# Optimization experiments

Measured on AMD Instinct MI355X. Metric: run time of the kernel, lower is better.

## Reference

```python
import jax, jax.numpy as jnp
import numpy as np

D_MODEL = 1024
NUM_HEADS = 16
D_HEAD = D_MODEL // NUM_HEADS


def setup_inputs() -> dict:
    key = jax.random.key(0)
    ks = jax.random.split(key, 9)
    s = 1.0 / np.sqrt(D_MODEL)
    return {
        "x": jax.random.normal(ks[0], (2, 2048, D_MODEL), dtype=jnp.float32),
        "Wq": jax.random.normal(ks[1], (D_MODEL, D_MODEL), dtype=jnp.float32) * s,
        "bq": jnp.zeros((D_MODEL,), dtype=jnp.float32),
        "Wk": jax.random.normal(ks[2], (D_MODEL, D_MODEL), dtype=jnp.float32) * s,
        "bk": jnp.zeros((D_MODEL,), dtype=jnp.float32),
        "Wv": jax.random.normal(ks[3], (D_MODEL, D_MODEL), dtype=jnp.float32) * s,
        "bv": jnp.zeros((D_MODEL,), dtype=jnp.float32),
        "Wo": jax.random.normal(ks[4], (D_MODEL, D_MODEL), dtype=jnp.float32) * s,
        "bo": jnp.zeros((D_MODEL,), dtype=jnp.float32),
    }


def reference(x, Wq, bq, Wk, bk, Wv, bv, Wo, bo):
    B, S, D = x.shape
    H, Dh = NUM_HEADS, D_HEAD

    def split_heads(t):  # [B,S,D] -> [B,H,S,Dh]
        return t.reshape(B, S, H, Dh).transpose(0, 2, 1, 3)

    # Linear layers: y = x @ W^T + b (torch nn.Linear convention)
    Q = split_heads(x @ Wq.T + bq)
    K = split_heads(x @ Wk.T + bk)
    V = split_heads(x @ Wv.T + bv)

    scale = 1.0 / jnp.sqrt(jnp.asarray(Dh, dtype=x.dtype))
    scores = jnp.einsum("bhqd,bhkd->bhqk", Q, K) * scale  # [B,H,S,S]
    attn = jax.nn.softmax(scores, axis=-1)
    context = jnp.einsum("bhqk,bhkd->bhqd", attn, V)  # [B,H,S,Dh]
    context = context.transpose(0, 2, 1, 3).reshape(B, S, D)
    return context @ Wo.T + bo
```

## Files before the change

kernel.cpp:

```cpp
#include <hip/hip_runtime.h>


#define T_TOK 4096
#define DM    1024
#define SQ    2048
#define NH    16
#define DH    64

typedef unsigned short u16;
typedef unsigned int   u32;
typedef __bf16 bf16x8 __attribute__((ext_vector_type(8)));
typedef float  f32x4  __attribute__((ext_vector_type(4)));
typedef float  f32x16 __attribute__((ext_vector_type(16)));
typedef u32    u32x4  __attribute__((ext_vector_type(4)));

__device__ __forceinline__ u16 f2bf(float f) {
  u32 u = __builtin_bit_cast(u32, f);
  u32 r = (u + 0x7FFFu + ((u >> 16) & 1u)) >> 16;
  return (u16)r;
}

#if __has_builtin(__builtin_amdgcn_cvt_pk_bf16_f32)
typedef __bf16 bf16x2 __attribute__((ext_vector_type(2)));
__device__ __forceinline__ u32 pk2bf(float a, float b) {
  bf16x2 h = __builtin_amdgcn_cvt_pk_bf16_f32(a, b);
  return __builtin_bit_cast(u32, h);
}
#else
__device__ __forceinline__ u32 pk2bf(float a, float b) {
  u32 r;
  asm("v_cvt_pk_bf16_f32 %0, %1, %2" : "=v"(r) : "v"(a), "v"(b));
  return r;
}
#endif

__device__ __forceinline__ void gld16(const void* g, void* l) {
  __builtin_amdgcn_global_load_lds(
      (const __attribute__((address_space(1))) u32*)g,
      (__attribute__((address_space(3))) u32*)l, 16, 0, 0);
}

__global__ void cast_bf16_kernel(const float* __restrict__ x,
    const float* __restrict__ w0, const float* __restrict__ w1,
    const float* __restrict__ w2, const float* __restrict__ w3,
    u16* __restrict__ xb, u16* __restrict__ o0, u16* __restrict__ o1,
    u16* __restrict__ o2, u16* __restrict__ o3)
{
  const float* src; u16* dst; int n;
  switch (blockIdx.y) {
    case 0:  src = x;  dst = xb; n = T_TOK * DM; break;
    case 1:  src = w0; dst = o0; n = DM * DM; break;
    case 2:  src = w1; dst = o1; n = DM * DM; break;
    case 3:  src = w2; dst = o2; n = DM * DM; break;
    default: src = w3; dst = o3; n = DM * DM; break;
  }
  const int stride = gridDim.x * blockDim.x;
  for (int i = blockIdx.x * blockDim.x + threadIdx.x; i * 4 < n; i += stride) {
    float4 v = ((const float4*)src)[i];
    ushort4 o;
    o.x = f2bf(v.x); o.y = f2bf(v.y); o.z = f2bf(v.z); o.w = f2bf(v.w);
    ((ushort4*)dst)[i] = o;
  }
}

__device__ __forceinline__ void gemm_core_128x128(
    u16* lds, const u16* __restrict__ Ab, const u16* __restrict__ Bb,
    f32x4 acc[4][4])
{
  u16* As = lds;
  u16* Bs = lds + 8192;
  const int tid = threadIdx.x, lane = tid & 63, w = tid >> 6;
  const int waveM = w >> 1, waveN = w & 1;
  const int col = lane & 15, quad = lane >> 4;
  const int srow = lane >> 3;
  const int sg0  = (lane & 7) ^ srow;

  for (int k0 = 0; k0 < DM; k0 += 64) {
    #pragma unroll
    for (int i = 0; i < 4; ++i) {
      const int rb = w * 32 + i * 8;
      const int sg = sg0 ^ ((rb >> 3) & 3);
      gld16(Ab + (size_t)(rb + srow) * DM + k0 + sg * 8, &As[rb * 64]);
      gld16(Bb + (size_t)(rb + srow) * DM + k0 + sg * 8, &Bs[rb * 64]);
    }
    __syncthreads();
    #pragma unroll
    for (int c = 0; c < 2; ++c) {
      bf16x8 af[4], bg[4];
      #pragma unroll
      for (int i = 0; i < 4; ++i) {
        const int row = waveM * 64 + i * 16 + col;
        const int gp = (c * 4 + quad) ^ (row & 7) ^ ((row >> 3) & 3);
        af[i] = *(const bf16x8*)&As[row * 64 + gp * 8];
      }
      #pragma unroll
      for (int j = 0; j < 4; ++j) {
        const int row = waveN * 64 + j * 16 + col;
        const int gp = (c * 4 + quad) ^ (row & 7) ^ ((row >> 3) & 3);
        bg[j] = *(const bf16x8*)&Bs[row * 64 + gp * 8];
      }
      #pragma unroll
      for (int i = 0; i < 4; ++i) {
        #pragma unroll
        for (int j = 0; j < 4; ++j)
          acc[i][j] = __builtin_amdgcn_mfma_f32_16x16x32_bf16(af[i], bg[j], acc[i][j], 0, 0, 0);
      }
    }
    __syncthreads();
  }
}

__device__ __forceinline__ void gemm_core_128x64(
    u16* lds, const u16* __restrict__ Ab, const u16* __restrict__ Bb,
    f32x4 acc[4][2])
{
  u16* As = lds;
  u16* Bs = lds + 8192;
  const int tid = threadIdx.x, lane = tid & 63, w = tid >> 6;
  const int waveM = w >> 1, waveN = w & 1;
  const int col = lane & 15, quad = lane >> 4;
  const int srow = lane >> 3;
  const int sg0  = (lane & 7) ^ srow;

  for (int k0 = 0; k0 < DM; k0 += 64) {
    #pragma unroll
    for (int i = 0; i < 4; ++i) {
      const int rb = w * 32 + i * 8;
      const int sg = sg0 ^ ((rb >> 3) & 3);
      gld16(Ab + (size_t)(rb + srow) * DM + k0 + sg * 8, &As[rb * 64]);
    }
    #pragma unroll
    for (int i = 0; i < 2; ++i) {
      const int rb = w * 16 + i * 8;
      const int sg = sg0 ^ ((rb >> 3) & 3);
      gld16(Bb + (size_t)(rb + srow) * DM + k0 + sg * 8, &Bs[rb * 64]);
    }
    __syncthreads();
    #pragma unroll
    for (int c = 0; c < 2; ++c) {
      bf16x8 af[4], bg[2];
      #pragma unroll
      for (int i = 0; i < 4; ++i) {
        const int row = waveM * 64 + i * 16 + col;
        const int gp = (c * 4 + quad) ^ (row & 7) ^ ((row >> 3) & 3);
        af[i] = *(const bf16x8*)&As[row * 64 + gp * 8];
      }
      #pragma unroll
      for (int j = 0; j < 2; ++j) {
        const int row = waveN * 32 + j * 16 + col;
        const int gp = (c * 4 + quad) ^ (row & 7) ^ ((row >> 3) & 3);
        bg[j] = *(const bf16x8*)&Bs[row * 64 + gp * 8];
      }
      #pragma unroll
      for (int i = 0; i < 4; ++i) {
        #pragma unroll
        for (int j = 0; j < 2; ++j)
          acc[i][j] = __builtin_amdgcn_mfma_f32_16x16x32_bf16(af[i], bg[j], acc[i][j], 0, 0, 0);
      }
    }
    __syncthreads();
  }
}

__global__ __launch_bounds__(256) void gemm_qkv_kernel(
    const u16* __restrict__ xb,
    const u16* __restrict__ Wqb, const u16* __restrict__ Wkb, const u16* __restrict__ Wvb,
    const float* __restrict__ bq, const float* __restrict__ bk, const float* __restrict__ bv,
    u16* __restrict__ Qs, u16* __restrict__ Kh, u16* __restrict__ Vt)
{
  __shared__ __align__(16) u16 smem[128 * 136];
  u16* tr = smem;
  const int z = blockIdx.z;
  const int tb = blockIdx.x;
  const int cb = blockIdx.y;
  const u16*   Wb   = (z == 0) ? Wqb : (z == 1) ? Wkb : Wvb;
  const float* bias = (z == 0) ? bq  : (z == 1) ? bk  : bv;
  const float scale = (z == 0) ? 0.18033688011112042f : 1.0f;

  const int tid = threadIdx.x;
  const int lane = tid & 63, w = tid >> 6;
  const int waveM = w >> 1, waveN = w & 1;
  const int col = lane & 15, quad = lane >> 4;
  const f32x4 zf = {0.f, 0.f, 0.f, 0.f};

  f32x4 acc[4][4];
  #pragma unroll
  for (int i = 0; i < 4; ++i) {
    #pragma unroll
    for (int j = 0; j < 4; ++j) acc[i][j] = zf;
  }

  if (z == 2) {
    gemm_core_128x128(smem, xb + (size_t)(tb * 128) * DM,
                      Wb + (size_t)(cb * 128) * DM, acc);
    #pragma unroll
    for (int j = 0; j < 4; ++j) {
      const int cl = waveN * 64 + j * 16 + col;
      const float bb = bias[cb * 128 + cl];
      #pragma unroll
      for (int i = 0; i < 4; ++i) {
        const int tl = waveM * 64 + i * 16 + quad * 4;
        ushort4 pk;
        pk.x = f2bf(acc[i][j][0] + bb); pk.y = f2bf(acc[i][j][1] + bb);
        pk.z = f2bf(acc[i][j][2] + bb); pk.w = f2bf(acc[i][j][3] + bb);
        *(ushort4*)&tr[cl * 136 + tl] = pk;
      }
    }
    __syncthreads();
    const int t0 = tb * 128;
    const int b = t0 >> 11, sBase = t0 & 2047;
    #pragma unroll
    for (int rep = 0; rep < 8; ++rep) {
      const int chunk = rep * 256 + tid;
      const int row = chunk >> 4, off = (chunk & 15) * 8;
      const int c = cb * 128 + row;
      const int h = c >> 6, d = c & 63;
      uint4 v = *(const uint4*)&tr[row * 136 + off];
      *(uint4*)&Vt[((size_t)(b * NH + h) * DH + d) * SQ + sBase + off] = v;
    }
  } else {
    gemm_core_128x128(smem, Wb + (size_t)(cb * 128) * DM,
                      xb + (size_t)(tb * 128) * DM, acc);
    u16* out = (z == 0) ? Qs : Kh;
    const int chBase  = cb * 128 + waveM * 64;
    const int tokBase = tb * 128 + waveN * 64;
    #pragma unroll
    for (int i = 0; i < 4; ++i) {
      const int c0 = chBase + i * 16 + quad * 4;
      const int hh = c0 >> 6, d0 = c0 & 63;
      const float4 bb = *(const float4*)&bias[c0];
      #pragma unroll
      for (int j = 0; j < 4; ++j) {
        const int t = tokBase + j * 16 + col;
        const int b = t >> 11, s = t & 2047;
        ushort4 pk;
        pk.x = f2bf((acc[i][j][0] + bb.x) * scale);
        pk.y = f2bf((acc[i][j][1] + bb.y) * scale);
        pk.z = f2bf((acc[i][j][2] + bb.z) * scale);
        pk.w = f2bf((acc[i][j][3] + bb.w) * scale);
        *(ushort4*)&out[((size_t)(b * NH + hh) * SQ + s) * DH + d0] = pk;
      }
    }
  }
}

__global__ __launch_bounds__(256, 4) void attn_kernel(
    const u16* __restrict__ Qs, const u16* __restrict__ Kh,
    const u16* __restrict__ Vt, u16* __restrict__ ctx)
{
  __shared__ __align__(16) char smem[33 * 1024];
  u16* KtB = (u16*)smem;
  u16* VlB = (u16*)(smem + 16384);
  f32x4* red  = (f32x4*)smem;
  float* lred = (float*)(smem + 32768);

  const int tid = threadIdx.x, lane = tid & 63, w = tid >> 6;
  const int l31 = lane & 31, h = lane >> 5;
  const int qt = w & 1, st = w >> 1;
  const int bh = blockIdx.x, q0 = blockIdx.y * 64;
  const u16* Qb = Qs + ((size_t)bh * SQ + q0) * DH;
  const u16* Kb = Kh + (size_t)bh * SQ * DH;
  const u16* Vb = Vt + (size_t)bh * DH * SQ;
  const int srow = lane >> 3;
  const int sgl  = (lane & 7) ^ srow;

  bf16x8 qreg[4];
  #pragma unroll
  for (int ks = 0; ks < 4; ++ks)
    qreg[ks] = *(const bf16x8*)(Qb + (size_t)(qt * 32 + l31) * DH + ks * 16 + h * 8);

  #pragma unroll
  for (int i = 0; i < 2; ++i) {
    const int rb = w * 16 + i * 8;
    const int sg = sgl ^ ((rb >> 3) & 3);
    gld16(Kb + (size_t)(rb + srow) * DH + sg * 8, &KtB[rb * 64]);
    gld16(Vb + (size_t)(rb + srow) * SQ + sg * 8, &VlB[rb * 64]);
  }

  f32x16 cacc[2];
  #pragma unroll
  for (int dt = 0; dt < 2; ++dt)
    #pragma unroll
    for (int e = 0; e < 16; ++e) cacc[dt][e] = 0.f;
  float l_s = 0.f;
  __syncthreads();

  for (int kt = 0; kt < SQ / 64; ++kt) {
    const int cur = kt & 1;
    u16* Kt = KtB + cur * 4096;
    u16* Vl = VlB + cur * 4096;
    if (kt + 1 < SQ / 64) {
      const int nxt = cur ^ 1, s1 = (kt + 1) * 64;
      u16* Ktn = KtB + nxt * 4096;
      u16* Vln = VlB + nxt * 4096;
      #pragma unroll
      for (int i = 0; i < 2; ++i) {
        const int rb = w * 16 + i * 8;
        const int sg = sgl ^ ((rb >> 3) & 3);
        gld16(Kb + (size_t)(s1 + rb + srow) * DH + sg * 8, &Ktn[rb * 64]);
        gld16(Vb + (size_t)(rb + srow) * SQ + s1 + sg * 8, &Vln[rb * 64]);
      }
    }

    f32x16 sacc;
    #pragma unroll
    for (int e = 0; e < 16; ++e) sacc[e] = 0.f;
    __builtin_amdgcn_s_setprio(1);
    #pragma unroll
    for (int ks = 0; ks < 4; ++ks) {
      const int row = st * 32 + l31;
      const int gp = (2 * ks + h) ^ (l31 & 7) ^ ((l31 >> 3) & 3);
      bf16x8 kf = *(const bf16x8*)&Kt[row * 64 + gp * 8];
      sacc = __builtin_amdgcn_mfma_f32_32x32x16_bf16(kf, qreg[ks], sacc, 0, 0, 0);
    }
    __builtin_amdgcn_s_setprio(0);

    u32 Pp[4][2];
    {
      float p[16];
      #pragma unroll
      for (int e = 0; e < 16; ++e)
        p[e] = __builtin_amdgcn_exp2f(sacc[e]);
      float t0 = (p[0] + p[1]) + (p[2] + p[3]);
      float t1 = (p[4] + p[5]) + (p[6] + p[7]);
      float t2 = (p[8] + p[9]) + (p[10] + p[11]);
      float t3 = (p[12] + p[13]) + (p[14] + p[15]);
      l_s += (t0 + t1) + (t2 + t3);
      #pragma unroll
      for (int rg = 0; rg < 4; ++rg) {
        Pp[rg][0] = pk2bf(p[4 * rg + 0], p[4 * rg + 1]);
        Pp[rg][1] = pk2bf(p[4 * rg + 2], p[4 * rg + 3]);
      }
    }

    __builtin_amdgcn_s_setprio(1);
    #pragma unroll
    for (int ks = 0; ks < 2; ++ks) {
      u32 own0 = h ? Pp[2 * ks + 1][0] : Pp[2 * ks][0];
      u32 own1 = h ? Pp[2 * ks + 1][1] : Pp[2 * ks][1];
      u32 snd0 = h ? Pp[2 * ks][0] : Pp[2 * ks + 1][0];
      u32 snd1 = h ? Pp[2 * ks][1] : Pp[2 * ks + 1][1];
      u32 rcv0 = (u32)__shfl_xor((int)snd0, 32, 64);
      u32 rcv1 = (u32)__shfl_xor((int)snd1, 32, 64);
      u32x4 fw;
      fw.x = h ? rcv0 : own0;
      fw.y = h ? rcv1 : own1;
      fw.z = h ? own0 : rcv0;
      fw.w = h ? own1 : rcv1;
      bf16x8 pf = __builtin_bit_cast(bf16x8, fw);
      #pragma unroll
      for (int dt = 0; dt < 2; ++dt) {
        const int row = dt * 32 + l31;
        const int gp = (4 * st + 2 * ks + h) ^ (l31 & 7) ^ ((l31 >> 3) & 3);
        bf16x8 vf = *(const bf16x8*)&Vl[row * 64 + gp * 8];
        cacc[dt] = __builtin_amdgcn_mfma_f32_32x32x16_bf16(vf, pf, cacc[dt], 0, 0, 0);
      }
    }
    __builtin_amdgcn_s_setprio(0);
    __syncthreads();
  }

  float lq = l_s + __shfl_xor(l_s, 32, 64);
  if (h == 0) lred[w * 32 + l31] = lq;
  #pragma unroll
  for (int dt = 0; dt < 2; ++dt) {
    #pragma unroll
    for (int c = 0; c < 4; ++c) {
      f32x4 ch;
      ch[0] = cacc[dt][4 * c + 0]; ch[1] = cacc[dt][4 * c + 1];
      ch[2] = cacc[dt][4 * c + 2]; ch[3] = cacc[dt][4 * c + 3];
      red[((w * 2 + dt) * 4 + c) * 64 + lane] = ch;
    }
  }
  __syncthreads();
  const int qt2 = w & 1, dt2 = w >> 1;
  const int b = bh >> 4, hd = bh & 15;
  const float lsum = lred[qt2 * 32 + l31] + lred[(2 + qt2) * 32 + l31];
  const float inv = 1.0f / lsum;
  const int s = q0 + qt2 * 32 + l31;
  #pragma unroll
  for (int c = 0; c < 4; ++c) {
    f32x4 sum = red[((qt2 * 2 + dt2) * 4 + c) * 64 + lane];
    sum += red[(((2 + qt2) * 2 + dt2) * 4 + c) * 64 + lane];
    const int d0 = dt2 * 32 + c * 8 + 4 * h;
    ushort4 pk;
    pk.x = f2bf(sum[0] * inv); pk.y = f2bf(sum[1] * inv);
    pk.z = f2bf(sum[2] * inv); pk.w = f2bf(sum[3] * inv);
    *(ushort4*)&ctx[(size_t)(b * SQ + s) * DM + hd * DH + d0] = pk;
  }
}

__global__ __launch_bounds__(256) void gemm_out_kernel(
    const u16* __restrict__ ctx, const u16* __restrict__ Wob,
    const float* __restrict__ bo, float* __restrict__ out)
{
  __shared__ __align__(16) u16 smem[128 * 64 + 64 * 64];
  const int tb = blockIdx.x;
  const int cb = blockIdx.y;
  const int tid = threadIdx.x, lane = tid & 63, w = tid >> 6;
  const int waveM = w >> 1, waveN = w & 1;
  const int col = lane & 15, quad = lane >> 4;

  f32x4 acc[4][2];
  const f32x4 zf = {0.f, 0.f, 0.f, 0.f};
  #pragma unroll
  for (int i = 0; i < 4; ++i) {
    #pragma unroll
    for (int j = 0; j < 2; ++j) acc[i][j] = zf;
  }

  gemm_core_128x64(smem, ctx + (size_t)(tb * 128) * DM,
                   Wob + (size_t)(cb * 64) * DM, acc);

  const int rowBase = tb * 128 + waveM * 64;
  const int colBase = cb * 64 + waveN * 32;
  #pragma unroll
  for (int j = 0; j < 2; ++j) {
    const int c = colBase + j * 16 + col;
    const float bb = bo[c];
    #pragma unroll
    for (int i = 0; i < 4; ++i) {
      #pragma unroll
      for (int r = 0; r < 4; ++r) {
        const int t = rowBase + i * 16 + quad * 4 + r;
        out[(size_t)t * DM + c] = acc[i][j][r] + bb;
      }
    }
  }
}

extern "C" void kernel_launch(void* const* d_in, const int* in_sizes, int n_in,
                              void* d_out, int out_size, void* d_ws, size_t ws_size,
                              hipStream_t stream) {
  const float* x  = (const float*)d_in[0];
  const float* Wq = (const float*)d_in[1];
  const float* bq = (const float*)d_in[2];
  const float* Wk = (const float*)d_in[3];
  const float* bk = (const float*)d_in[4];
  const float* Wv = (const float*)d_in[5];
  const float* bv = (const float*)d_in[6];
  const float* Wo = (const float*)d_in[7];
  const float* bo = (const float*)d_in[8];

  char* ws = (char*)d_ws;
  u16* xb  = (u16*)(ws);
  u16* Wqb = (u16*)(ws + (8ull  << 20));
  u16* Wkb = (u16*)(ws + (10ull << 20));
  u16* Wvb = (u16*)(ws + (12ull << 20));
  u16* Wob = (u16*)(ws + (14ull << 20));
  u16* Qs  = (u16*)(ws + (16ull << 20));
  u16* Kh  = (u16*)(ws + (24ull << 20));
  u16* Vt  = (u16*)(ws + (32ull << 20));
  u16* ctx = xb;

  cast_bf16_kernel<<<dim3(256, 5), 256, 0, stream>>>(x, Wq, Wk, Wv, Wo,
                                                     xb, Wqb, Wkb, Wvb, Wob);
  gemm_qkv_kernel<<<dim3(32, 8, 3), 256, 0, stream>>>(xb, Wqb, Wkb, Wvb,
                                                      bq, bk, bv, Qs, Kh, Vt);
  attn_kernel<<<dim3(32, 32), 256, 0, stream>>>(Qs, Kh, Vt, ctx);
  gemm_out_kernel<<<dim3(32, 16), 256, 0, stream>>>(ctx, Wob, bo, (float*)d_out);
  (void)in_sizes; (void)n_in; (void)out_size; (void)ws_size;
}
```

Baseline: 199.9 us.

## Load K/V fragments directly from global memory and use permlane32 swap

The attention kernel no longer stages K and V tiles through double-buffered shared memory. Each wave now loads its K and V MFMA fragments straight from global memory into registers, which removes the LDS copies and the per-iteration __syncthreads. The P-fragment exchange between wave halves now uses v_permlane32_swap in place of shuffles and selects. The trade-off is that every wave fetches its own fragments without prefetch overlap, so latency is exposed and the same K/V data is reloaded by multiple waves, relying on the caches.

Measured after the change: 270.0 us. 1.35x slower.

```diff
diff --git a/kernel.cpp b/kernel.cpp
--- a/kernel.cpp
+++ b/kernel.cpp
@@ -249,8 +249,6 @@
     const u16* __restrict__ Vt, u16* __restrict__ ctx)
 {
   __shared__ __align__(16) char smem[33 * 1024];
-  u16* KtB = (u16*)smem;
-  u16* VlB = (u16*)(smem + 16384);
   f32x4* red  = (f32x4*)smem;
   float* lred = (float*)(smem + 32768);
 
@@ -261,21 +259,15 @@
   const u16* Qb = Qs + ((size_t)bh * SQ + q0) * DH;
   const u16* Kb = Kh + (size_t)bh * SQ * DH;
   const u16* Vb = Vt + (size_t)bh * DH * SQ;
-  const int srow = lane >> 3;
-  const int sgl  = (lane & 7) ^ srow;
 
   bf16x8 qreg[4];
   #pragma unroll
   for (int ks = 0; ks < 4; ++ks)
     qreg[ks] = *(const bf16x8*)(Qb + (size_t)(qt * 32 + l31) * DH + ks * 16 + h * 8);
 
-  #pragma unroll
-  for (int i = 0; i < 2; ++i) {
-    const int rb = w * 16 + i * 8;
-    const int sg = sgl ^ ((rb >> 3) & 3);
-    gld16(Kb + (size_t)(rb + srow) * DH + sg * 8, &KtB[rb * 64]);
-    gld16(Vb + (size_t)(rb + srow) * SQ + sg * 8, &VlB[rb * 64]);
-  }
+  const u16* Kp  = Kb + (size_t)(st * 32 + l31) * DH + h * 8;
+  const u16* Vp0 = Vb + (size_t)l31 * SQ        + st * 32 + h * 8;
+  const u16* Vp1 = Vb + (size_t)(32 + l31) * SQ + st * 32 + h * 8;
 
   f32x16 cacc[2];
   #pragma unroll
@@ -283,36 +275,24 @@
     #pragma unroll
     for (int e = 0; e < 16; ++e) cacc[dt][e] = 0.f;
   float l_s = 0.f;
-  __syncthreads();
 
   for (int kt = 0; kt < SQ / 64; ++kt) {
-    const int cur = kt & 1;
-    u16* Kt = KtB + cur * 4096;
-    u16* Vl = VlB + cur * 4096;
-    if (kt + 1 < SQ / 64) {
-      const int nxt = cur ^ 1, s1 = (kt + 1) * 64;
-      u16* Ktn = KtB + nxt * 4096;
-      u16* Vln = VlB + nxt * 4096;
-      #pragma unroll
-      for (int i = 0; i < 2; ++i) {
-        const int rb = w * 16 + i * 8;
-        const int sg = sgl ^ ((rb >> 3) & 3);
-        gld16(Kb + (size_t)(s1 + rb + srow) * DH + sg * 8, &Ktn[rb * 64]);
-        gld16(Vb + (size_t)(rb + srow) * SQ + s1 + sg * 8, &Vln[rb * 64]);
-      }
-    }
-
-    f32x16 sacc;
-    #pragma unroll
-    for (int e = 0; e < 16; ++e) sacc[e] = 0.f;
+    bf16x8 kf0  = *(const bf16x8*)(Kp +  0);
+    bf16x8 kf1  = *(const bf16x8*)(Kp + 16);
+    bf16x8 kf2  = *(const bf16x8*)(Kp + 32);
+    bf16x8 kf3  = *(const bf16x8*)(Kp + 48);
+    bf16x8 vf00 = *(const bf16x8*)(Vp0 +  0);
+    bf16x8 vf01 = *(const bf16x8*)(Vp0 + 16);
+    bf16x8 vf10 = *(const bf16x8*)(Vp1 +  0);
+    bf16x8 vf11 = *(const bf16x8*)(Vp1 + 16);
+    Kp += 64 * DH; Vp0 += 64; Vp1 += 64;
+
+    f32x16 sacc = {};
     __builtin_amdgcn_s_setprio(1);
-    #pragma unroll
-    for (int ks = 0; ks < 4; ++ks) {
-      const int row = st * 32 + l31;
-      const int gp = (2 * ks + h) ^ (l31 & 7) ^ ((l31 >> 3) & 3);
-      bf16x8 kf = *(const bf16x8*)&Kt[row * 64 + gp * 8];
-      sacc = __builtin_amdgcn_mfma_f32_32x32x16_bf16(kf, qreg[ks], sacc, 0, 0, 0);
-    }
+    sacc = __builtin_amdgcn_mfma_f32_32x32x16_bf16(kf0, qreg[0], sacc, 0, 0, 0);
+    sacc = __builtin_amdgcn_mfma_f32_32x32x16_bf16(kf1, qreg[1], sacc, 0, 0, 0);
+    sacc = __builtin_amdgcn_mfma_f32_32x32x16_bf16(kf2, qreg[2], sacc, 0, 0, 0);
+    sacc = __builtin_amdgcn_mfma_f32_32x32x16_bf16(kf3, qreg[3], sacc, 0, 0, 0);
     __builtin_amdgcn_s_setprio(0);
 
     u32 Pp[4][2];
@@ -336,28 +316,17 @@
     __builtin_amdgcn_s_setprio(1);
     #pragma unroll
     for (int ks = 0; ks < 2; ++ks) {
-      u32 own0 = h ? Pp[2 * ks + 1][0] : Pp[2 * ks][0];
-      u32 own1 = h ? Pp[2 * ks + 1][1] : Pp[2 * ks][1];
-      u32 snd0 = h ? Pp[2 * ks][0] : Pp[2 * ks + 1][0];
-      u32 snd1 = h ? Pp[2 * ks][1] : Pp[2 * ks + 1][1];
-      u32 rcv0 = (u32)__shfl_xor((int)snd0, 32, 64);
-      u32 rcv1 = (u32)__shfl_xor((int)snd1, 32, 64);
+      u32 a0 = Pp[2 * ks][0], b0 = Pp[2 * ks + 1][0];
+      u32 a1 = Pp[2 * ks][1], b1 = Pp[2 * ks + 1][1];
+      asm("v_permlane32_swap_b32 %0, %1" : "+v"(a0), "+v"(b0));
+      asm("v_permlane32_swap_b32 %0, %1" : "+v"(a1), "+v"(b1));
       u32x4 fw;
-      fw.x = h ? rcv0 : own0;
-      fw.y = h ? rcv1 : own1;
-      fw.z = h ? own0 : rcv0;
-      fw.w = h ? own1 : rcv1;
+      fw.x = a0; fw.y = a1; fw.z = b0; fw.w = b1;
       bf16x8 pf = __builtin_bit_cast(bf16x8, fw);
-      #pragma unroll
-      for (int dt = 0; dt < 2; ++dt) {
-        const int row = dt * 32 + l31;
-        const int gp = (4 * st + 2 * ks + h) ^ (l31 & 7) ^ ((l31 >> 3) & 3);
-        bf16x8 vf = *(const bf16x8*)&Vl[row * 64 + gp * 8];
-        cacc[dt] = __builtin_amdgcn_mfma_f32_32x32x16_bf16(vf, pf, cacc[dt], 0, 0, 0);
-      }
+      cacc[0] = __builtin_amdgcn_mfma_f32_32x32x16_bf16(ks ? vf01 : vf00, pf, cacc[0], 0, 0, 0);
+      cacc[1] = __builtin_amdgcn_mfma_f32_32x32x16_bf16(ks ? vf11 : vf10, pf, cacc[1], 0, 0, 0);
     }
     __builtin_amdgcn_s_setprio(0);
-    __syncthreads();
   }
 
   float lq = l_s + __shfl_xor(l_s, 32, 64);
```

## Fuse Q and K projections into one block sharing the x tile

Applied to the files above, without the earlier changes.

The QKV projection kernel now computes Q and K together in one block, loading each x tile once and reusing it for two weight tiles with two accumulator sets. The grid shrinks from three z-slices to two (QK fused, V separate), and launch bounds are set to 2 blocks per CU. This cuts redundant global/LDS loads of x. In exchange it doubles accumulator registers per thread and makes the QK blocks about twice as long as the V blocks, so work is unevenly balanced across the grid.

Measured after the change: 188.8 us. 1.06x faster.

```diff
diff --git a/kernel.cpp b/kernel.cpp
--- a/kernel.cpp
+++ b/kernel.cpp
@@ -110,12 +110,13 @@
   }
 }
 
-__device__ __forceinline__ void gemm_core_128x64(
-    u16* lds, const u16* __restrict__ Ab, const u16* __restrict__ Bb,
-    f32x4 acc[4][2])
+__device__ __forceinline__ void gemm_core_qk(
+    u16* lds, const u16* __restrict__ Aq, const u16* __restrict__ Ak,
+    const u16* __restrict__ Bb, f32x4 accQ[4][4], f32x4 accK[4][4])
 {
   u16* As = lds;
-  u16* Bs = lds + 8192;
+  u16* A2 = lds + 8192;
+  u16* Bs = lds + 16384;
   const int tid = threadIdx.x, lane = tid & 63, w = tid >> 6;
   const int waveM = w >> 1, waveN = w & 1;
   const int col = lane & 15, quad = lane >> 4;
@@ -127,55 +128,51 @@
     for (int i = 0; i < 4; ++i) {
       const int rb = w * 32 + i * 8;
       const int sg = sg0 ^ ((rb >> 3) & 3);
-      gld16(Ab + (size_t)(rb + srow) * DM + k0 + sg * 8, &As[rb * 64]);
-    }
-    #pragma unroll
-    for (int i = 0; i < 2; ++i) {
-      const int rb = w * 16 + i * 8;
-      const int sg = sg0 ^ ((rb >> 3) & 3);
-      gld16(Bb + (size_t)(rb + srow) * DM + k0 + sg * 8, &Bs[rb * 64]);
+      const size_t off = (size_t)(rb + srow) * DM + k0 + sg * 8;
+      gld16(Aq + off, &As[rb * 64]);
+      gld16(Ak + off, &A2[rb * 64]);
+      gld16(Bb + off, &Bs[rb * 64]);
     }
     __syncthreads();
     #pragma unroll
     for (int c = 0; c < 2; ++c) {
-      bf16x8 af[4], bg[2];
+      bf16x8 af[4], ag[4], bg[4];
       #pragma unroll
       for (int i = 0; i < 4; ++i) {
         const int row = waveM * 64 + i * 16 + col;
         const int gp = (c * 4 + quad) ^ (row & 7) ^ ((row >> 3) & 3);
         af[i] = *(const bf16x8*)&As[row * 64 + gp * 8];
-      }
-      #pragma unroll
-      for (int j = 0; j < 2; ++j) {
-        const int row = waveN * 32 + j * 16 + col;
+        ag[i] = *(const bf16x8*)&A2[row * 64 + gp * 8];
+      }
+      #pragma unroll
+      for (int j = 0; j < 4; ++j) {
+        const int row = waveN * 64 + j * 16 + col;
         const int gp = (c * 4 + quad) ^ (row & 7) ^ ((row >> 3) & 3);
         bg[j] = *(const bf16x8*)&Bs[row * 64 + gp * 8];
       }
       #pragma unroll
       for (int i = 0; i < 4; ++i) {
         #pragma unroll
-        for (int j = 0; j < 2; ++j)
-          acc[i][j] = __builtin_amdgcn_mfma_f32_16x16x32_bf16(af[i], bg[j], acc[i][j], 0, 0, 0);
-      }
-    }
-    __syncthreads();
-  }
-}
-
-__global__ __launch_bounds__(256) void gemm_qkv_kernel(
+        for (int j = 0; j < 4; ++j) {
+          accQ[i][j] = __builtin_amdgcn_mfma_f32_16x16x32_bf16(af[i], bg[j], accQ[i][j], 0, 0, 0);
+          accK[i][j] = __builtin_amdgcn_mfma_f32_16x16x32_bf16(ag[i], bg[j], accK[i][j], 0, 0, 0);
+        }
+      }
+    }
+    __syncthreads();
+  }
+}
+
+__global__ __launch_bounds__(256, 2) void gemm_qkv_kernel(
     const u16* __restrict__ xb,
     const u16* __restrict__ Wqb, const u16* __restrict__ Wkb, const u16* __restrict__ Wvb,
     const float* __restrict__ bq, const float* __restrict__ bk, const float* __restrict__ bv,
     u16* __restrict__ Qs, u16* __restrict__ Kh, u16* __restrict__ Vt)
 {
-  __shared__ __align__(16) u16 smem[128 * 136];
-  u16* tr = smem;
+  __shared__ __align__(16) u16 smem[3 * 8192];
   const int z = blockIdx.z;
   const int tb = blockIdx.x;
   const int cb = blockIdx.y;
-  const u16*   Wb   = (z == 0) ? Wqb : (z == 1) ? Wkb : Wvb;
-  const float* bias = (z == 0) ? bq  : (z == 1) ? bk  : bv;
-  const float scale = (z == 0) ? 0.18033688011112042f : 1.0f;
 
   const int tid = threadIdx.x;
   const int lane = tid & 63, w = tid >> 6;
@@ -183,20 +180,19 @@
   const int col = lane & 15, quad = lane >> 4;
   const f32x4 zf = {0.f, 0.f, 0.f, 0.f};
 
-  f32x4 acc[4][4];
-  #pragma unroll
-  for (int i = 0; i < 4; ++i) {
-    #pragma unroll
-    for (int j = 0; j < 4; ++j) acc[i][j] = zf;
-  }
-
-  if (z == 2) {
+  if (z == 1) {
+    u16* tr = smem;
+    f32x4 acc[4][4];
+    #pragma unroll
+    for (int i = 0; i < 4; ++i)
+      #pragma unroll
+      for (int j = 0; j < 4; ++j) acc[i][j] = zf;
     gemm_core_128x128(smem, xb + (size_t)(tb * 128) * DM,
-                      Wb + (size_t)(cb * 128) * DM, acc);
+                      Wvb + (size_t)(cb * 128) * DM, acc);
     #pragma unroll
     for (int j = 0; j < 4; ++j) {
       const int cl = waveN * 64 + j * 16 + col;
-      const float bb = bias[cb * 128 + cl];
+      const float bb = bv[cb * 128 + cl];
       #pragma unroll
       for (int i = 0; i < 4; ++i) {
         const int tl = waveM * 64 + i * 16 + quad * 4;
@@ -219,26 +215,40 @@
       *(uint4*)&Vt[((size_t)(b * NH + h) * DH + d) * SQ + sBase + off] = v;
     }
   } else {
-    gemm_core_128x128(smem, Wb + (size_t)(cb * 128) * DM,
-                      xb + (size_t)(tb * 128) * DM, acc);
-    u16* out = (z == 0) ? Qs : Kh;
+    f32x4 accQ[4][4], accK[4][4];
+    #pragma unroll
+    for (int i = 0; i < 4; ++i)
+      #pragma unroll
+      for (int j = 0; j < 4; ++j) { accQ[i][j] = zf; accK[i][j] = zf; }
+    gemm_core_qk(smem, Wqb + (size_t)(cb * 128) * DM,
+                 Wkb + (size_t)(cb * 128) * DM,
+                 xb + (size_t)(tb * 128) * DM, accQ, accK);
+    const float qscale = 0.18033688011112042f;
     const int chBase  = cb * 128 + waveM * 64;
     const int tokBase = tb * 128 + waveN * 64;
     #pragma unroll
     for (int i = 0; i < 4; ++i) {
       const int c0 = chBase + i * 16 + quad * 4;
       const int hh = c0 >> 6, d0 = c0 & 63;
-      const float4 bb = *(const float4*)&bias[c0];
+      const float4 bbq = *(const float4*)&bq[c0];
+      const float4 bbk = *(const float4*)&bk[c0];
       #pragma unroll
       for (int j = 0; j < 4; ++j) {
         const int t = tokBase + j * 16 + col;
         const int b = t >> 11, s = t & 2047;
+        const size_t base = ((size_t)(b * NH + hh) * SQ + s) * DH + d0;
+        ushort4 pq;
+        pq.x = f2bf((accQ[i][j][0] + bbq.x) * qscale);
+        pq.y = f2bf((accQ[i][j][1] + bbq.y) * qscale);
+        pq.z = f2bf((accQ[i][j][2] + bbq.z) * qscale);
+        pq.w = f2bf((accQ[i][j][3] + bbq.w) * qscale);
+        *(ushort4*)&Qs[base] = pq;
         ushort4 pk;
-        pk.x = f2bf((acc[i][j][0] + bb.x) * scale);
-        pk.y = f2bf((acc[i][j][1] + bb.y) * scale);
-        pk.z = f2bf((acc[i][j][2] + bb.z) * scale);
-        pk.w = f2bf((acc[i][j][3] + bb.w) * scale);
-        *(ushort4*)&out[((size_t)(b * NH + hh) * SQ + s) * DH + d0] = pk;
+        pk.x = f2bf(accK[i][j][0] + bbk.x);
+        pk.y = f2bf(accK[i][j][1] + bbk.y);
+        pk.z = f2bf(accK[i][j][2] + bbk.z);
+        pk.w = f2bf(accK[i][j][3] + bbk.w);
+        *(ushort4*)&Kh[base] = pk;
       }
     }
   }
@@ -390,6 +400,58 @@
   }
 }
 
+__device__ __forceinline__ void gemm_core_128x64(
+    u16* lds, const u16* __restrict__ Ab, const u16* __restrict__ Bb,
+    f32x4 acc[4][2])
+{
+  u16* As = lds;
+  u16* Bs = lds + 8192;
+  const int tid = threadIdx.x, lane = tid & 63, w = tid >> 6;
+  const int waveM = w >> 1, waveN = w & 1;
+  const int col = lane & 15, quad = lane >> 4;
+  const int srow = lane >> 3;
+  const int sg0  = (lane & 7) ^ srow;
+
+  for (int k0 = 0; k0 < DM; k0 += 64) {
+    #pragma unroll
+    for (int i = 0; i < 4; ++i) {
+      const int rb = w * 32 + i * 8;
+      const int sg = sg0 ^ ((rb >> 3) & 3);
+      gld16(Ab + (size_t)(rb + srow) * DM + k0 + sg * 8, &As[rb * 64]);
+    }
+    #pragma unroll
+    for (int i = 0; i < 2; ++i) {
+      const int rb = w * 16 + i * 8;
+      const int sg = sg0 ^ ((rb >> 3) & 3);
+      gld16(Bb + (size_t)(rb + srow) * DM + k0 + sg * 8, &Bs[rb * 64]);
+    }
+    __syncthreads();
+    #pragma unroll
+    for (int c = 0; c < 2; ++c) {
+      bf16x8 af[4], bg[2];
+      #pragma unroll
+      for (int i = 0; i < 4; ++i) {
+        const int row = waveM * 64 + i * 16 + col;
+        const int gp = (c * 4 + quad) ^ (row & 7) ^ ((row >> 3) & 3);
+        af[i] = *(const bf16x8*)&As[row * 64 + gp * 8];
+      }
+      #pragma unroll
+      for (int j = 0; j < 2; ++j) {
+        const int row = waveN * 32 + j * 16 + col;
+        const int gp = (c * 4 + quad) ^ (row & 7) ^ ((row >> 3) & 3);
+        bg[j] = *(const bf16x8*)&Bs[row * 64 + gp * 8];
+      }
+      #pragma unroll
+      for (int i = 0; i < 4; ++i) {
+        #pragma unroll
+        for (int j = 0; j < 2; ++j)
+          acc[i][j] = __builtin_amdgcn_mfma_f32_16x16x32_bf16(af[i], bg[j], acc[i][j], 0, 0, 0);
+      }
+    }
+    __syncthreads();
+  }
+}
+
 __global__ __launch_bounds__(256) void gemm_out_kernel(
     const u16* __restrict__ ctx, const u16* __restrict__ Wob,
     const float* __restrict__ bo, float* __restrict__ out)
@@ -455,7 +517,7 @@
 
   cast_bf16_kernel<<<dim3(256, 5), 256, 0, stream>>>(x, Wq, Wk, Wv, Wo,
                                                      xb, Wqb, Wkb, Wvb, Wob);
-  gemm_qkv_kernel<<<dim3(32, 8, 3), 256, 0, stream>>>(xb, Wqb, Wkb, Wvb,
+  gemm_qkv_kernel<<<dim3(32, 8, 2), 256, 0, stream>>>(xb, Wqb, Wkb, Wvb,
                                                       bq, bk, bv, Qs, Kh, Vt);
   attn_kernel<<<dim3(32, 32), 256, 0, stream>>>(Qs, Kh, Vt, ctx);
   gemm_out_kernel<<<dim3(32, 16), 256, 0, stream>>>(ctx, Wob, bo, (float*)d_out);
```
